# Kernel optimization log

Measured on AMD Instinct MI355X. Metric: run time of the kernel, lower is better.

## Reference

```python
import jax, jax.numpy as jnp
import numpy as np

K = 3          # conv kernel size
STRIDE = 1     # conv stride (SAME padding)
ITERS = 3      # DR routing iterations
EPS = 1e-9     # squash epsilon


def squash(s, axis):
    # v = ||s||^2 / (1 + ||s||^2) * s / ||s||   (DR squash)
    sq = jnp.sum(s * s, axis=axis, keepdims=True)
    return (sq / (1.0 + sq)) * s * jax.lax.rsqrt(sq + EPS)


def setup_inputs() -> dict:
    key = jax.random.key(0)
    k1, k2, k3 = jax.random.split(key, 3)
    b, h, w, iCaps, iPose = 8, 12, 12, 32, 16
    oCaps, oPose = 32, 16
    x = jax.random.normal(k1, (b, h, w, iCaps, iPose), dtype=jnp.float32)
    # Wa: [kk*iCaps, oCaps, iPose, oPose] (leading 1 of the TF weight is dropped)
    fan = K * K * iCaps * iPose
    W = jax.random.normal(k2, (K * K * iCaps, oCaps, iPose, oPose), dtype=jnp.float32) * np.float32(np.sqrt(2.0 / fan))
    # biases: [oCaps, oPose] (TF shape [1,1,oCaps,oPose,1], broadcastable)
    biases = jax.random.normal(k3, (oCaps, oPose), dtype=jnp.float32) * 0.05
    return {"x": x, "W": W, "biases": biases}


def _kernel_tile(x2d):
    # im2col for SAME padding, stride 1.  x2d: (b, h, w, C) -> (b, h, w, k*k, C)
    b, h, w, C = x2d.shape
    pad = K // 2
    xp = jnp.pad(x2d, ((0, 0), (pad, pad), (pad, pad), (0, 0)))
    patches = jnp.stack(
        [xp[:, i:i + h, j:j + w, :] for i in range(K) for j in range(K)], axis=3
    )
    return patches  # (b, h, w, k*k, C)


def reference(x, W, biases):
    b, h, w, iCaps, iPose = x.shape
    iC = K * K * iCaps
    oC, oP = biases.shape

    # 1. kernel_tile: gather k*k neighborhoods
    patches = _kernel_tile(x.reshape(b, h, w, iCaps * iPose))      # (b,h,w,kk,iCaps*iPose)
    u = patches.reshape(b * h * w, iC, iPose)                       # (bx, iC, iPose)

    # 2. transform_view (vector capsules): votes[n,i,c,:] = u[n,i,:] @ W[i,c,:,:]
    votes = jnp.einsum('nip,icpq->nicq', u, W)                      # (bx, iC, oC, oP)

    # 3. DR routing
    bx = votes.shape[0]
    logits = jnp.zeros((bx, iC, oC), dtype=votes.dtype)
    v = None
    for ii in range(ITERS):
        c = jax.nn.softmax(logits, axis=2)                          # coupling coeffs over oCaps
        s = jnp.einsum('nic,nicq->ncq', c, votes) + biases          # (bx, oC, oP)
        v = squash(s, axis=2)
        if ii < ITERS - 1:
            logits = logits + jnp.einsum('nicq,ncq->nic', votes, v)  # agreement

    return v.reshape(b, h, w, oC, oP)
```

## Files before the change

kernel.cpp:

```cpp
#include <hip/hip_runtime.h>
#include <stdint.h>

typedef unsigned short ushort_t;

#define KK3 3
#define IC 32
#define IP 16
#define OC 32
#define OP 16
#define NI 288
#define HH 12
#define WWW 12
#define NTOT 1152
#define CQ 512
#define EPSQ 1e-9f
#define RWAVES 4
#define RSTEPS 36
#define NIP 144
#define NIG 18
#define IPG 8

typedef __attribute__((ext_vector_type(8))) short bf16x8;
typedef __attribute__((ext_vector_type(4))) float f32x4;

__device__ __forceinline__ float bf_lo(unsigned u) { return __uint_as_float(u << 16); }
__device__ __forceinline__ float bf_hi(unsigned u) { return __uint_as_float(u & 0xffff0000u); }
__device__ __forceinline__ ushort_t f2bf(float f) {
    unsigned u = __float_as_uint(f);
    return (ushort_t)((u + 0x7fffu + ((u >> 16) & 1u)) >> 16);
}

__global__ __launch_bounds__(64) void pack_kernel(
    const float* __restrict__ W, ushort_t* __restrict__ Wp)
{
    const int blk = blockIdx.x;
    const int ip = blk >> 5;
    const int c = blk & 31;
    const int l = threadIdx.x;
    const int i = ip * 2 + ((l >> 5) & 1);
    const int p0 = ((l >> 4) & 1) * 8;
    const int q = l & 15;
    const float* src = W + (((size_t)(i * 32 + c) * 16 + p0) * 16 + q);
    union { ushort_t s[8]; uint4 u4; } o;
#pragma unroll
    for (int j = 0; j < 8; ++j) o.s[j] = f2bf(src[(size_t)j * 16]);
    *(uint4*)(Wp + ((size_t)blk * 64 + l) * 8) = o.u4;
}

__global__ __launch_bounds__(256) void votes_s0_kernel(
    const float* __restrict__ x, const ushort_t* __restrict__ Wp,
    ushort_t* __restrict__ votes, float* __restrict__ s0_part,
    int nStart, int nCount)
{
    __shared__ float slab[2][16][CQ];

    const int t = threadIdx.x;
    const int w = t >> 6;
    const int l = t & 63;
    const int pxt = blockIdx.x;
    const int ig = blockIdx.y;

    const int n = nStart + pxt * 16 + (l & 15);
    const int b = n / (HH * WWW);
    const int rem = n % (HH * WWW);
    const int y = rem / WWW;
    const int xx = rem % WWW;
    const int ioff = (l >> 5) & 1;
    const int p0 = ((l >> 4) & 1) * 8;

    const bf16x8 z8 = {0, 0, 0, 0, 0, 0, 0, 0};
    const f32x4 z4 = {0.f, 0.f, 0.f, 0.f};

    f32x4 accs0[8];
#pragma unroll
    for (int ctl = 0; ctl < 8; ++ctl) accs0[ctl] = z4;

    for (int m = 0; m < IPG; ++m) {
        const int ip = ig * IPG + m;
        union { ushort_t s[8]; bf16x8 v; } ua;
        {
            const int i = ip * 2 + ioff;
            const int ky = i / (KK3 * IC);
            const int kx = (i / IC) % KK3;
            const int ic = i & (IC - 1);
            const int sy = y + ky - 1;
            const int sx = xx + kx - 1;
            if (sy >= 0 && sy < HH && sx >= 0 && sx < WWW) {
                const float* s = x + ((((size_t)b * HH + sy) * WWW + sx) * IC + ic) * IP + p0;
                const float4 v0 = *(const float4*)s;
                const float4 v1 = *(const float4*)(s + 4);
                ua.s[0] = f2bf(v0.x); ua.s[1] = f2bf(v0.y); ua.s[2] = f2bf(v0.z); ua.s[3] = f2bf(v0.w);
                ua.s[4] = f2bf(v1.x); ua.s[5] = f2bf(v1.y); ua.s[6] = f2bf(v1.z); ua.s[7] = f2bf(v1.w);
            } else {
#pragma unroll
                for (int j = 0; j < 8; ++j) ua.s[j] = 0;
            }
        }
        const int q = l & 15;
        const int r0 = (l >> 4) * 4;
#pragma unroll
        for (int ctl = 0; ctl < 8; ++ctl) {
            const int ct = w * 8 + ctl;
            const bf16x8 frag = *(const bf16x8*)(Wp + (((size_t)ip * 32 + ct) * 64 + l) * 8);
            const bf16x8 be = (l < 32) ? frag : z8;
            const bf16x8 bo = (l < 32) ? z8 : frag;
            const f32x4 ve = __builtin_amdgcn_mfma_f32_16x16x32_bf16(ua.v, be, z4, 0, 0, 0);
            const f32x4 vo = __builtin_amdgcn_mfma_f32_16x16x32_bf16(ua.v, bo, z4, 0, 0, 0);
            accs0[ctl] = __builtin_amdgcn_mfma_f32_16x16x32_bf16(ua.v, frag, accs0[ctl], 0, 0, 0);
            const int col = ct * 16 + q;
#pragma unroll
            for (int r = 0; r < 4; ++r) {
                slab[0][r0 + r][col] = ve[r];
                slab[1][r0 + r][col] = vo[r];
            }
        }
        __syncthreads();
        {
            const int px = t >> 4;
            const int ch0 = t & 15;
            const int nl = pxt * 16 + px;
#pragma unroll
            for (int s = 0; s < 2; ++s) {
                ushort_t* dst = votes + ((size_t)nl * NI + (2 * ip + s)) * CQ;
#pragma unroll
                for (int cc = 0; cc < 4; ++cc) {
                    const int ch = ch0 + cc * 16;
                    const float* sp = &slab[s][px][ch * 8];
                    const float4 f0 = *(const float4*)sp;
                    const float4 f1 = *(const float4*)(sp + 4);
                    union { ushort_t s8[8]; uint4 u4; } o;
                    o.s8[0] = f2bf(f0.x); o.s8[1] = f2bf(f0.y); o.s8[2] = f2bf(f0.z); o.s8[3] = f2bf(f0.w);
                    o.s8[4] = f2bf(f1.x); o.s8[5] = f2bf(f1.y); o.s8[6] = f2bf(f1.z); o.s8[7] = f2bf(f1.w);
                    *(uint4*)(dst + ch * 8) = o.u4;
                }
            }
        }
        __syncthreads();
    }

    {
        const int q = l & 15;
        const int r0 = (l >> 4) * 4;
#pragma unroll
        for (int ctl = 0; ctl < 8; ++ctl) {
            const int cq = (w * 8 + ctl) * 16 + q;
#pragma unroll
            for (int r = 0; r < 4; ++r)
                s0_part[((size_t)ig * nCount + pxt * 16 + r0 + r) * CQ + cq] = accs0[ctl][r];
        }
    }
}

__global__ __launch_bounds__(256) void s0_fin_kernel(
    const float* __restrict__ s0_part, float* __restrict__ s0_pre,
    int nStart, int nCount)
{
    const int bn = blockIdx.x;
    const int t = threadIdx.x;
#pragma unroll
    for (int rep = 0; rep < 2; ++rep) {
        const int k = t + rep * 256;
        float s = 0.f;
#pragma unroll
        for (int g = 0; g < NIG; ++g)
            s += s0_part[((size_t)g * nCount + bn) * CQ + k];
        s0_pre[(size_t)(nStart + bn) * CQ + k] = s;
    }
}

#define UNPACK16(A, B)                                                     \
    const float f0 = bf_lo(A.x), f1 = bf_hi(A.x), f2 = bf_lo(A.y),         \
                f3 = bf_hi(A.y), f4 = bf_lo(A.z), f5 = bf_hi(A.z),         \
                f6 = bf_lo(A.w), f7 = bf_hi(A.w), f8 = bf_lo(B.x),         \
                f9 = bf_hi(B.x), f10 = bf_lo(B.y), f11 = bf_hi(B.y),       \
                f12 = bf_lo(B.z), f13 = bf_hi(B.z), f14 = bf_lo(B.w),      \
                f15 = bf_hi(B.w);

__global__ __launch_bounds__(256) void route_kernel(
    const ushort_t* __restrict__ votes, const float* __restrict__ s0_pre,
    const float* __restrict__ bias, float* __restrict__ out, int nStart)
{
    __shared__ float lg_lds[NI * OC];
    __shared__ float sPart[RWAVES][CQ];
    __shared__ float s_sh[CQ];
    __shared__ float v_sh[CQ];
    __shared__ float fac_sh[OC];

    const int bn = blockIdx.x;
    const int t = threadIdx.x;
    const int wv = t >> 6;
    const int l = t & 63;
    const int isub = l >> 5;
    const int c = l & 31;
    const int iBase = 2 * wv + isub;

    const ushort_t* pbase = votes + (size_t)bn * NI * CQ + (size_t)iBase * CQ + c * OP;
    const size_t stepB = (size_t)8 * CQ;

#pragma unroll
    for (int rep = 0; rep < 2; ++rep) {
        const int k = t + rep * 256;
        s_sh[k] = fmaf(s0_pre[(size_t)(nStart + bn) * CQ + k], 1.0f / OC, bias[k]);
    }
    __syncthreads();
    if (t < OC) {
        float sq = 0.f;
#pragma unroll
        for (int q = 0; q < OP; ++q) { const float s = s_sh[t * OP + q]; sq = fmaf(s, s, sq); }
        fac_sh[t] = (sq / (1.0f + sq)) * rsqrtf(sq + EPSQ);
    }
    __syncthreads();
#pragma unroll
    for (int rep = 0; rep < 2; ++rep) {
        const int k = t + rep * 256;
        v_sh[k] = s_sh[k] * fac_sh[k >> 4];
    }
    __syncthreads();

    float sa[16];
    float vr[16];

#define RBODY(AA, BB, rr)                                                   \
        {                                                                   \
            UNPACK16(AA, BB)                                                \
            float a = f0 * vr[0];                                           \
            a = fmaf(f1, vr[1], a);   a = fmaf(f2, vr[2], a);               \
            a = fmaf(f3, vr[3], a);   a = fmaf(f4, vr[4], a);               \
            a = fmaf(f5, vr[5], a);   a = fmaf(f6, vr[6], a);               \
            a = fmaf(f7, vr[7], a);   a = fmaf(f8, vr[8], a);               \
            a = fmaf(f9, vr[9], a);   a = fmaf(f10, vr[10], a);             \
            a = fmaf(f11, vr[11], a); a = fmaf(f12, vr[12], a);             \
            a = fmaf(f13, vr[13], a); a = fmaf(f14, vr[14], a);             \
            a = fmaf(f15, vr[15], a);                                       \
            const int li = (iBase + 8 * (rr)) * OC + c;                     \
            if (it == 0) lg_lds[li] = a;                                    \
            else          a += lg_lds[li];                                  \
            const float e = __expf(a);                                      \
            float es = e;                                                   \
            es += __shfl_xor(es, 1);                                        \
            es += __shfl_xor(es, 2);                                        \
            es += __shfl_xor(es, 4);                                        \
            es += __shfl_xor(es, 8);                                        \
            es += __shfl_xor(es, 16);                                       \
            const float coup = __fdividef(e, es);                           \
            sa[0] = fmaf(coup, f0, sa[0]);   sa[1] = fmaf(coup, f1, sa[1]); \
            sa[2] = fmaf(coup, f2, sa[2]);   sa[3] = fmaf(coup, f3, sa[3]); \
            sa[4] = fmaf(coup, f4, sa[4]);   sa[5] = fmaf(coup, f5, sa[5]); \
            sa[6] = fmaf(coup, f6, sa[6]);   sa[7] = fmaf(coup, f7, sa[7]); \
            sa[8] = fmaf(coup, f8, sa[8]);   sa[9] = fmaf(coup, f9, sa[9]); \
            sa[10] = fmaf(coup, f10, sa[10]); sa[11] = fmaf(coup, f11, sa[11]); \
            sa[12] = fmaf(coup, f12, sa[12]); sa[13] = fmaf(coup, f13, sa[13]); \
            sa[14] = fmaf(coup, f14, sa[14]); sa[15] = fmaf(coup, f15, sa[15]); \
        }
#define RPREF(AA, BB, rn)                                                   \
        if ((rn) < RSTEPS) {                                                \
            const uint4* pn = (const uint4*)(pbase + (size_t)(rn) * stepB); \
            AA = pn[0]; BB = pn[1];                                         \
        }

#pragma unroll
    for (int it = 0; it < 2; ++it) {
#pragma unroll
        for (int k = 0; k < 4; ++k) {
            const float4 v4 = *(const float4*)&v_sh[c * 16 + 4 * k];
            vr[4*k] = v4.x; vr[4*k+1] = v4.y; vr[4*k+2] = v4.z; vr[4*k+3] = v4.w;
        }
#pragma unroll
        for (int q = 0; q < 16; ++q) sa[q] = 0.f;

        uint4 A0, B0, A1, B1, A2, B2;
        RPREF(A0, B0, 0)
        RPREF(A1, B1, 1)
        RPREF(A2, B2, 2)
        for (int r = 0; r < RSTEPS; r += 3) {
            RBODY(A0, B0, r)     RPREF(A0, B0, r + 3)
            RBODY(A1, B1, r + 1) RPREF(A1, B1, r + 4)
            RBODY(A2, B2, r + 2) RPREF(A2, B2, r + 5)
        }

#pragma unroll
        for (int q = 0; q < 16; ++q) sa[q] += __shfl_xor(sa[q], 32);
        if (isub == 0) {
#pragma unroll
            for (int k = 0; k < 4; ++k)
                *(float4*)&sPart[wv][c * 16 + 4 * k] = make_float4(sa[4*k], sa[4*k+1], sa[4*k+2], sa[4*k+3]);
        }
        __syncthreads();
#pragma unroll
        for (int rep = 0; rep < 2; ++rep) {
            const int k = t + rep * 256;
            float s = (sPart[0][k] + sPart[1][k]) + (sPart[2][k] + sPart[3][k]);
            s_sh[k] = s + bias[k];
        }
        __syncthreads();
        if (t < OC) {
            float sq = 0.f;
#pragma unroll
            for (int q = 0; q < OP; ++q) { const float s = s_sh[t * OP + q]; sq = fmaf(s, s, sq); }
            fac_sh[t] = (sq / (1.0f + sq)) * rsqrtf(sq + EPSQ);
        }
        __syncthreads();
#pragma unroll
        for (int rep = 0; rep < 2; ++rep) {
            const int k = t + rep * 256;
            v_sh[k] = s_sh[k] * fac_sh[k >> 4];
        }
        __syncthreads();
    }

#pragma unroll
    for (int rep = 0; rep < 2; ++rep) {
        const int k = t + rep * 256;
        out[(size_t)(nStart + bn) * CQ + k] = v_sh[k];
    }
}

extern "C" void kernel_launch(void* const* d_in, const int* in_sizes, int n_in,
                              void* d_out, int out_size, void* d_ws, size_t ws_size,
                              hipStream_t stream)
{
    const float* x = (const float*)d_in[0];
    const float* Wg = (const float*)d_in[1];
    const float* bias = (const float*)d_in[2];
    float* out = (float*)d_out;

    const size_t perN = (size_t)NI * CQ * sizeof(ushort_t);
    const size_t packBytes = (size_t)NIP * 32 * 64 * 8 * 2;
    const size_t s0Bytes = (size_t)NTOT * CQ * sizeof(float);
    const size_t perNpart = (size_t)NIG * CQ * sizeof(float);

    int chunk = 768;
    if (ws_size < (size_t)chunk * (perN + perNpart) + packBytes + s0Bytes) {
        size_t avail = (ws_size > packBytes + s0Bytes) ? ws_size - packBytes - s0Bytes : 0;
        chunk = (int)(avail / (perN + perNpart));
        chunk &= ~15;
        if (chunk < 16) chunk = 16;
    }
    const size_t packOff = (size_t)chunk * perN;
    const size_t s0Off = packOff + packBytes;
    const size_t partOff = s0Off + s0Bytes;

    ushort_t* votes = (ushort_t*)d_ws;
    ushort_t* Wp = (ushort_t*)((char*)d_ws + packOff);
    float* s0_pre = (float*)((char*)d_ws + s0Off);
    float* s0_part = (float*)((char*)d_ws + partOff);

    hipLaunchKernelGGL(pack_kernel, dim3(NIP * 32), dim3(64), 0, stream, Wg, Wp);

    for (int start = 0; start < NTOT; start += chunk) {
        const int cnt = (NTOT - start < chunk) ? (NTOT - start) : chunk;
        hipLaunchKernelGGL(votes_s0_kernel, dim3(cnt / 16, NIG), dim3(256), 0, stream,
                           x, Wp, votes, s0_part, start, cnt);
        hipLaunchKernelGGL(s0_fin_kernel, dim3(cnt), dim3(256), 0, stream,
                           s0_part, s0_pre, start, cnt);
        hipLaunchKernelGGL(route_kernel, dim3(cnt), dim3(256), 0, stream,
                           votes, s0_pre, bias, out, start);
    }
}
```

Before: 215.0 us.

## Store votes directly from MFMA registers and deepen routing prefetch

The votes kernel stops staging MFMA outputs through a shared-memory slab and drops both __syncthreads per iteration. Each lane now converts its results to bf16 and writes them straight to global memory as scattered 2-byte stores. The routing loop's software prefetch depth grows from 3 to 6 steps, and partial-tile bounds handling is added for chunk counts that are not multiples of 16. The direct stores remove shared-memory traffic and barriers but give up the 16-byte coalesced stores, and the deeper prefetch uses more registers.

New measurement: 250.0 us. 1.16x slower.

```diff
diff --git a/kernel.cpp b/kernel.cpp
--- a/kernel.cpp
+++ b/kernel.cpp
@@ -52,21 +52,23 @@
     ushort_t* __restrict__ votes, float* __restrict__ s0_part,
     int nStart, int nCount)
 {
-    __shared__ float slab[2][16][CQ];
-
     const int t = threadIdx.x;
     const int w = t >> 6;
     const int l = t & 63;
     const int pxt = blockIdx.x;
     const int ig = blockIdx.y;
 
-    const int n = nStart + pxt * 16 + (l & 15);
+    const int pxa = pxt * 16 + (l & 15);
+    const int n = nStart + ((pxa < nCount) ? pxa : 0);
     const int b = n / (HH * WWW);
     const int rem = n % (HH * WWW);
     const int y = rem / WWW;
     const int xx = rem % WWW;
     const int ioff = (l >> 5) & 1;
     const int p0 = ((l >> 4) & 1) * 8;
+
+    const int q = l & 15;
+    const int r0 = (l >> 4) * 4;
 
     const bf16x8 z8 = {0, 0, 0, 0, 0, 0, 0, 0};
     const f32x4 z4 = {0.f, 0.f, 0.f, 0.f};
@@ -96,8 +98,16 @@
                 for (int j = 0; j < 8; ++j) ua.s[j] = 0;
             }
         }
-        const int q = l & 15;
-        const int r0 = (l >> 4) * 4;
+        ushort_t* be_ptr[4];
+        ushort_t* bo_ptr[4];
+#pragma unroll
+        for (int r = 0; r < 4; ++r) {
+            const size_t nl = (size_t)(pxt * 16 + r0 + r);
+            be_ptr[r] = votes + (nl * NI + 2 * ip) * CQ + w * 128 + q;
+            bo_ptr[r] = be_ptr[r] + CQ;
+        }
+        const bool rowOK = (pxt * 16 + r0 + 3 < nCount) | (nCount % 16 == 0);
+
 #pragma unroll
         for (int ctl = 0; ctl < 8; ++ctl) {
             const int ct = w * 8 + ctl;
@@ -107,46 +117,26 @@
             const f32x4 ve = __builtin_amdgcn_mfma_f32_16x16x32_bf16(ua.v, be, z4, 0, 0, 0);
             const f32x4 vo = __builtin_amdgcn_mfma_f32_16x16x32_bf16(ua.v, bo, z4, 0, 0, 0);
             accs0[ctl] = __builtin_amdgcn_mfma_f32_16x16x32_bf16(ua.v, frag, accs0[ctl], 0, 0, 0);
-            const int col = ct * 16 + q;
-#pragma unroll
-            for (int r = 0; r < 4; ++r) {
-                slab[0][r0 + r][col] = ve[r];
-                slab[1][r0 + r][col] = vo[r];
-            }
-        }
-        __syncthreads();
-        {
-            const int px = t >> 4;
-            const int ch0 = t & 15;
-            const int nl = pxt * 16 + px;
-#pragma unroll
-            for (int s = 0; s < 2; ++s) {
-                ushort_t* dst = votes + ((size_t)nl * NI + (2 * ip + s)) * CQ;
-#pragma unroll
-                for (int cc = 0; cc < 4; ++cc) {
-                    const int ch = ch0 + cc * 16;
-                    const float* sp = &slab[s][px][ch * 8];
-                    const float4 f0 = *(const float4*)sp;
-                    const float4 f1 = *(const float4*)(sp + 4);
-                    union { ushort_t s8[8]; uint4 u4; } o;
-                    o.s8[0] = f2bf(f0.x); o.s8[1] = f2bf(f0.y); o.s8[2] = f2bf(f0.z); o.s8[3] = f2bf(f0.w);
-                    o.s8[4] = f2bf(f1.x); o.s8[5] = f2bf(f1.y); o.s8[6] = f2bf(f1.z); o.s8[7] = f2bf(f1.w);
-                    *(uint4*)(dst + ch * 8) = o.u4;
+            if (rowOK) {
+#pragma unroll
+                for (int r = 0; r < 4; ++r) {
+                    be_ptr[r][ctl * 16] = f2bf(ve[r]);
+                    bo_ptr[r][ctl * 16] = f2bf(vo[r]);
                 }
             }
         }
-        __syncthreads();
     }
 
     {
-        const int q = l & 15;
-        const int r0 = (l >> 4) * 4;
 #pragma unroll
         for (int ctl = 0; ctl < 8; ++ctl) {
             const int cq = (w * 8 + ctl) * 16 + q;
 #pragma unroll
-            for (int r = 0; r < 4; ++r)
-                s0_part[((size_t)ig * nCount + pxt * 16 + r0 + r) * CQ + cq] = accs0[ctl][r];
+            for (int r = 0; r < 4; ++r) {
+                const int px = pxt * 16 + r0 + r;
+                if (px < nCount)
+                    s0_part[((size_t)ig * nCount + px) * CQ + cq] = accs0[ctl][r];
+            }
         }
     }
 }
@@ -268,14 +258,20 @@
 #pragma unroll
         for (int q = 0; q < 16; ++q) sa[q] = 0.f;
 
-        uint4 A0, B0, A1, B1, A2, B2;
+        uint4 A0, B0, A1, B1, A2, B2, A3, B3, A4, B4, A5, B5;
         RPREF(A0, B0, 0)
         RPREF(A1, B1, 1)
         RPREF(A2, B2, 2)
-        for (int r = 0; r < RSTEPS; r += 3) {
-            RBODY(A0, B0, r)     RPREF(A0, B0, r + 3)
-            RBODY(A1, B1, r + 1) RPREF(A1, B1, r + 4)
-            RBODY(A2, B2, r + 2) RPREF(A2, B2, r + 5)
+        RPREF(A3, B3, 3)
+        RPREF(A4, B4, 4)
+        RPREF(A5, B5, 5)
+        for (int r = 0; r < RSTEPS; r += 6) {
+            RBODY(A0, B0, r)     RPREF(A0, B0, r + 6)
+            RBODY(A1, B1, r + 1) RPREF(A1, B1, r + 7)
+            RBODY(A2, B2, r + 2) RPREF(A2, B2, r + 8)
+            RBODY(A3, B3, r + 3) RPREF(A3, B3, r + 9)
+            RBODY(A4, B4, r + 4) RPREF(A4, B4, r + 10)
+            RBODY(A5, B5, r + 5) RPREF(A5, B5, r + 11)
         }
 
 #pragma unroll
@@ -349,7 +345,7 @@
 
     for (int start = 0; start < NTOT; start += chunk) {
         const int cnt = (NTOT - start < chunk) ? (NTOT - start) : chunk;
-        hipLaunchKernelGGL(votes_s0_kernel, dim3(cnt / 16, NIG), dim3(256), 0, stream,
+        hipLaunchKernelGGL(votes_s0_kernel, dim3((cnt + 15) / 16, NIG), dim3(256), 0, stream,
                            x, Wp, votes, s0_part, start, cnt);
         hipLaunchKernelGGL(s0_fin_kernel, dim3(cnt), dim3(256), 0, stream,
                            s0_part, s0_pre, start, cnt);
```
